# Kernel tuning notes

Measured on AMD Instinct MI355X. Metric: run time of the kernel, lower is better.

Reference implementation:

```python
import jax, jax.numpy as jnp
import numpy as np

K = 2  # top-k experts per token


def setup_inputs() -> dict:
    key = jax.random.key(0)
    k1, k2 = jax.random.split(key)
    B, T, D, E = 4, 4096, 4096, 64
    x = jax.random.normal(k1, (B, T, D), dtype=jnp.float32)
    W = jax.random.normal(k2, (E, D), dtype=jnp.float32) * (1.0 / np.sqrt(D))
    return {"x": x, "W": W}


def reference(x, W):
    # router_logits: [B, T, E]  (nn.Linear with no bias: x @ W.T)
    router_logits = jnp.einsum('btd,ed->bte', x, W)
    # top-k over expert dim, then softmax over the k selected logits
    topk_logits, topk_idx = jax.lax.top_k(router_logits, K)  # [B,T,K]
    topk_weight = jax.nn.softmax(topk_logits, axis=-1)       # [B,T,K]
    return (topk_idx, topk_weight, router_logits)
```

## Files before the change

### kernel.cpp

```cpp
#include <hip/hip_runtime.h>
#include <math.h>

#define NTOK 16384
#define DDIM 4096
#define NEXP 64
#define TAU  2e-4f
#define WS_LO 262144
#define NCW  32

typedef short bf16x8 __attribute__((ext_vector_type(8)));
typedef float f32x4  __attribute__((ext_vector_type(4)));

__device__ __forceinline__ unsigned short bf16_rne(float f) {
  unsigned u = __float_as_uint(f);
  u += 0x7fffu + ((u >> 16) & 1u);
  return (unsigned short)(u >> 16);
}

__device__ __forceinline__ void split4(float4 v, uint2& hi, uint2& lo) {
  unsigned h0 = bf16_rne(v.x), h1 = bf16_rne(v.y), h2 = bf16_rne(v.z), h3 = bf16_rne(v.w);
  float r0 = v.x - __uint_as_float(h0 << 16);
  float r1 = v.y - __uint_as_float(h1 << 16);
  float r2 = v.z - __uint_as_float(h2 << 16);
  float r3 = v.w - __uint_as_float(h3 << 16);
  unsigned l0 = bf16_rne(r0), l1 = bf16_rne(r1), l2 = bf16_rne(r2), l3 = bf16_rne(r3);
  hi = make_uint2(h0 | (h1 << 16), h2 | (h3 << 16));
  lo = make_uint2(l0 | (l1 << 16), l2 | (l3 << 16));
}

__device__ __forceinline__ void split4v(f32x4 v, uint2& hi, uint2& lo) {
  unsigned h0 = bf16_rne(v[0]), h1 = bf16_rne(v[1]), h2 = bf16_rne(v[2]), h3 = bf16_rne(v[3]);
  float r0 = v[0] - __uint_as_float(h0 << 16);
  float r1 = v[1] - __uint_as_float(h1 << 16);
  float r2 = v[2] - __uint_as_float(h2 << 16);
  float r3 = v[3] - __uint_as_float(h3 << 16);
  unsigned l0 = bf16_rne(r0), l1 = bf16_rne(r1), l2 = bf16_rne(r2), l3 = bf16_rne(r3);
  hi = make_uint2(h0 | (h1 << 16), h2 | (h3 << 16));
  lo = make_uint2(l0 | (l1 << 16), l2 | (l3 << 16));
}

__device__ __forceinline__ bf16x8 mk8(uint2 a, uint2 b) {
  union { uint4 u; bf16x8 v; } t;
  t.u = make_uint4(a.x, a.y, b.x, b.y);
  return t.v;
}

__device__ __forceinline__ void gld_lds16(const float* g, char* l) {
  __builtin_amdgcn_global_load_lds((const __attribute__((address_space(1))) void*)g,
                                   (__attribute__((address_space(3))) void*)l,
                                   16, 0, 0);
}

__device__ __forceinline__ bool better(float va, int ia, float vb, int ib) {
  return (va > vb) || (va == vb && ia < ib);
}
__device__ __forceinline__ bool betterd(double va, int ia, double vb, int ib) {
  return (va > vb) || (va == vb && ia < ib);
}
#define CE(va, ia, vb, ib) { if (better(vb, ib, va, ia)) { float _tv = va; va = vb; vb = _tv; int _ti = ia; ia = ib; ib = _ti; } }

__global__ __launch_bounds__(256)
void presplit_w(const float* __restrict__ w, short* __restrict__ ws) {
  const int tid = blockIdx.x * 256 + threadIdx.x;
  const int e = tid >> 9;
  const int o = tid & 511;
  const int c = o >> 2, q = o & 3;
  const int l = (e & 15) + 16 * q;
  const int g = e >> 4;
  const float* src = w + (size_t)e * DDIM + o * 8;
  float4 v0 = *(const float4*)src;
  float4 v1 = *(const float4*)(src + 4);
  uint2 h0, s0, h1, s1;
  split4(v0, h0, s0);
  split4(v1, h1, s1);
  const int off = c * 2048 + g * 512 + l * 8;
  *(uint4*)(ws + off)         = make_uint4(h0.x, h0.y, h1.x, h1.y);
  *(uint4*)(ws + WS_LO + off) = make_uint4(s0.x, s0.y, s1.x, s1.y);
}

__device__ __noinline__ void fixup_token(const float* __restrict__ x,
                                         const float* __restrict__ wgt,
                                         float* __restrict__ out_idx,
                                         float* __restrict__ out_wt,
                                         int tok, unsigned pk, int l) {
  const int e0 = pk & 255, e1 = (pk >> 8) & 255, e2 = (pk >> 16) & 255, e3 = (pk >> 24) & 255;
  const float* xr = x   + (size_t)tok * DDIM + l * 64;
  const float* w0 = wgt + (size_t)e0 * DDIM + l * 64;
  const float* w1 = wgt + (size_t)e1 * DDIM + l * 64;
  const float* w2 = wgt + (size_t)e2 * DDIM + l * 64;
  const float* w3 = wgt + (size_t)e3 * DDIM + l * 64;
  double s0 = 0.0, s1 = 0.0, s2 = 0.0, s3 = 0.0;
#pragma unroll 4
  for (int j = 0; j < 64; j += 4) {
    float4 xv = *(const float4*)(xr + j);
    float4 av = *(const float4*)(w0 + j);
    s0 = fma((double)xv.x, (double)av.x, s0); s0 = fma((double)xv.y, (double)av.y, s0);
    s0 = fma((double)xv.z, (double)av.z, s0); s0 = fma((double)xv.w, (double)av.w, s0);
    av = *(const float4*)(w1 + j);
    s1 = fma((double)xv.x, (double)av.x, s1); s1 = fma((double)xv.y, (double)av.y, s1);
    s1 = fma((double)xv.z, (double)av.z, s1); s1 = fma((double)xv.w, (double)av.w, s1);
    av = *(const float4*)(w2 + j);
    s2 = fma((double)xv.x, (double)av.x, s2); s2 = fma((double)xv.y, (double)av.y, s2);
    s2 = fma((double)xv.z, (double)av.z, s2); s2 = fma((double)xv.w, (double)av.w, s2);
    av = *(const float4*)(w3 + j);
    s3 = fma((double)xv.x, (double)av.x, s3); s3 = fma((double)xv.y, (double)av.y, s3);
    s3 = fma((double)xv.z, (double)av.z, s3); s3 = fma((double)xv.w, (double)av.w, s3);
  }
#pragma unroll
  for (int m = 1; m < 64; m <<= 1) {
    s0 += __shfl_xor(s0, m);
    s1 += __shfl_xor(s1, m);
    s2 += __shfl_xor(s2, m);
    s3 += __shfl_xor(s3, m);
  }
  if (l == 0) {
    double v0 = s0, v1 = s1, v2 = s2, v3 = s3;
    int i0 = e0, i1 = e1, i2 = e2, i3 = e3;
    if (betterd(v1, i1, v0, i0)) { double tv = v0; v0 = v1; v1 = tv; int ti = i0; i0 = i1; i1 = ti; }
    if (betterd(v3, i3, v2, i2)) { double tv = v2; v2 = v3; v3 = tv; int ti = i2; i2 = i3; i3 = ti; }
    if (betterd(v2, i2, v0, i0)) { double tv = v0; v0 = v2; v2 = tv; int ti = i0; i0 = i2; i2 = ti; }
    if (betterd(v3, i3, v1, i1)) { double tv = v1; v1 = v3; v3 = tv; int ti = i1; i1 = i3; i3 = ti; }
    if (betterd(v2, i2, v1, i1)) { double tv = v1; v1 = v2; v2 = tv; int ti = i1; i1 = i2; i2 = ti; }
    double ex = exp(v1 - v0);
    double den = 1.0 + ex;
    out_idx[tok * 2 + 0] = (float)i0;
    out_idx[tok * 2 + 1] = (float)i1;
    out_wt[tok * 2 + 0]  = (float)(1.0 / den);
    out_wt[tok * 2 + 1]  = (float)(ex / den);
  }
}

__global__ __launch_bounds__(256, 3)
void router_main(const float* __restrict__ x, const float* __restrict__ wgt,
                 const short* __restrict__ ws, float* __restrict__ out) {
  __shared__ __align__(16) char ldsbuf[32768];

  const int u = threadIdx.x;
  const int l = u & 63;
  const int wid = u >> 6;
  const int tokBase = blockIdx.x * 16;

  char* ring = ldsbuf + wid * 8192;
  const unsigned ldsbase =
      (unsigned)(size_t)(__attribute__((address_space(3))) char*)&ldsbuf[0];
  const unsigned rbase = ldsbase + wid * 8192 + l * 16;

  const int P = (blockIdx.x * 13) & 31;
#define PHYS(T) (((T) + P) & 31)

  const float* xbA = x + (size_t)(tokBase + (l & 15)) * DDIM + wid * 1024 + (l >> 4) * 8;
  const float* xbB = xbA + 4;

  const short* wch = ws + wid * 65536 + l * 8;

  f32x4 acc0 = {0,0,0,0}, acc1 = {0,0,0,0}, acc2 = {0,0,0,0}, acc3 = {0,0,0,0};
  bf16x8 wset[2][8];

#define LDW(SET, CC)                                                           \
  { asm volatile("" ::: "memory");                                             \
    wset[SET][0] = *(const bf16x8*)(wch + (CC) * 2048 + 0 * 512);              \
    wset[SET][1] = *(const bf16x8*)(wch + WS_LO + (CC) * 2048 + 0 * 512);      \
    wset[SET][2] = *(const bf16x8*)(wch + (CC) * 2048 + 1 * 512);              \
    wset[SET][3] = *(const bf16x8*)(wch + WS_LO + (CC) * 2048 + 1 * 512);      \
    wset[SET][4] = *(const bf16x8*)(wch + (CC) * 2048 + 2 * 512);              \
    wset[SET][5] = *(const bf16x8*)(wch + WS_LO + (CC) * 2048 + 2 * 512);      \
    wset[SET][6] = *(const bf16x8*)(wch + (CC) * 2048 + 3 * 512);              \
    wset[SET][7] = *(const bf16x8*)(wch + WS_LO + (CC) * 2048 + 3 * 512);      \
    asm volatile("" ::: "memory"); }

#define XISSUE(T, SLOT)                                                        \
  { const int cx_ = ((T) < NCW) ? (T) : NCW - 1;                               \
    const int cp_ = PHYS(cx_) * 32;                                            \
    char* d_ = ring + (SLOT) * 2048;                                           \
    gld_lds16(xbA + cp_, d_);                                                  \
    gld_lds16(xbB + cp_, d_ + 1024); }

#define MM(G, SET)                                                             \
  acc##G = __builtin_amdgcn_mfma_f32_16x16x32_bf16(ahi, wset[SET][2*(G)],   acc##G, 0, 0, 0); \
  acc##G = __builtin_amdgcn_mfma_f32_16x16x32_bf16(ahi, wset[SET][2*(G)+1], acc##G, 0, 0, 0); \
  acc##G = __builtin_amdgcn_mfma_f32_16x16x32_bf16(alo, wset[SET][2*(G)],   acc##G, 0, 0, 0);

#define STEP(T, SLOT, SET)                                                     \
  {                                                                            \
    asm volatile("" ::: "memory");                                             \
    XISSUE((T) + 3, ((T) + 3) & 3)                                             \
    asm volatile("s_waitcnt vmcnt(14)" ::: "memory");                          \
    {                                                                          \
      f32x4 f0, f1;                                                            \
      unsigned a_ = rbase + (SLOT) * 2048;                                     \
      asm volatile("ds_read_b128 %0, %2\n\tds_read_b128 %1, %2 offset:1024"    \
                   : "=&v"(f0), "=&v"(f1) : "v"(a_));                          \
      asm volatile("s_waitcnt lgkmcnt(0)" ::: "memory");                       \
      __builtin_amdgcn_sched_barrier(0);                                       \
      uint2 h0_, s0_, h1_, s1_;                                                \
      split4v(f0, h0_, s0_); split4v(f1, h1_, s1_);                            \
      bf16x8 ahi = mk8(h0_, h1_), alo = mk8(s0_, s1_);                         \
      MM(0, SET) MM(1, SET) MM(2, SET) MM(3, SET)                              \
    }                                                                          \
    { const int cw_ = ((T) + 2 < NCW) ? (T) + 2 : NCW - 1;                     \
      LDW(SET, PHYS(cw_)) }                                                    \
  }

  XISSUE(0, 0)
  LDW(0, PHYS(0))
  XISSUE(1, 1)
  LDW(1, PHYS(1))
  XISSUE(2, 2)

  for (int t = 0; t < NCW; t += 4) {
    STEP(t + 0, 0, 0)
    STEP(t + 1, 1, 1)
    STEP(t + 2, 2, 0)
    STEP(t + 3, 3, 1)
  }

  __syncthreads();
  float* p = (float*)ldsbuf;
#define PIDX(KQ, G, R) (((((KQ) * 4 + (G)) * 4 + (R)) << 6) + l)
  {
#pragma unroll
    for (int r = 0; r < 4; ++r) {
      p[PIDX(wid, 0, r)] = acc0[r];
      p[PIDX(wid, 1, r)] = acc1[r];
      p[PIDX(wid, 2, r)] = acc2[r];
      p[PIDX(wid, 3, r)] = acc3[r];
    }
  }
  __syncthreads();

  float* out_idx = out;
  float* out_wt  = out + NTOK * 2;
  float* out_lg  = out + NTOK * 4;

  float v0 = p[PIDX(0, 0, wid)] + p[PIDX(1, 0, wid)] + p[PIDX(2, 0, wid)] + p[PIDX(3, 0, wid)];
  float v1 = p[PIDX(0, 1, wid)] + p[PIDX(1, 1, wid)] + p[PIDX(2, 1, wid)] + p[PIDX(3, 1, wid)];
  float v2 = p[PIDX(0, 2, wid)] + p[PIDX(1, 2, wid)] + p[PIDX(2, 2, wid)] + p[PIDX(3, 2, wid)];
  float v3 = p[PIDX(0, 3, wid)] + p[PIDX(1, 3, wid)] + p[PIDX(2, 3, wid)] + p[PIDX(3, 3, wid)];

  const int tok = tokBase + (l >> 4) * 4 + wid;
  {
    float* dst = out_lg + (size_t)tok * NEXP + (l & 15);
    dst[0]  = v0;
    dst[16] = v1;
    dst[32] = v2;
    dst[48] = v3;
  }

  const int cbase = (l & 15);
  int i0 = cbase, i1 = cbase + 16, i2 = cbase + 32, i3 = cbase + 48;
  CE(v0, i0, v1, i1) CE(v2, i2, v3, i3) CE(v0, i0, v2, i2) CE(v1, i1, v3, i3) CE(v1, i1, v2, i2)
#pragma unroll
  for (int m = 1; m <= 8; m <<= 1) {
    float p0 = __shfl_xor(v0, m), p1 = __shfl_xor(v1, m);
    float p2 = __shfl_xor(v2, m), p3 = __shfl_xor(v3, m);
    int j0 = __shfl_xor(i0, m), j1 = __shfl_xor(i1, m);
    int j2 = __shfl_xor(i2, m), j3 = __shfl_xor(i3, m);
    CE(v0, i0, p3, j3) CE(v1, i1, p2, j2) CE(v2, i2, p1, j1) CE(v3, i3, p0, j0)
    CE(v0, i0, v2, i2) CE(v1, i1, v3, i3) CE(v0, i0, v1, i1) CE(v2, i2, v3, i3)
  }

  bool flag = false;
  unsigned pk = 0;
  if (cbase == 0) {
    flag = (v0 - v1 < TAU) || (v1 - v2 < TAU) || (v2 - v3 < TAU);
    pk = (unsigned)i0 | ((unsigned)i1 << 8) | ((unsigned)i2 << 16) | ((unsigned)i3 << 24);
    if (!flag) {
      float ex = expf(v1 - v0);
      float den = 1.0f + ex;
      out_idx[tok * 2 + 0] = (float)i0;
      out_idx[tok * 2 + 1] = (float)i1;
      out_wt[tok * 2 + 0]  = 1.0f / den;
      out_wt[tok * 2 + 1]  = ex / den;
    }
  }
  unsigned long long mk = __ballot(flag);
  while (mk) {
    const int src = __builtin_ctzll(mk);
    mk &= mk - 1;
    const unsigned pks = (unsigned)__shfl((int)pk, src);
    fixup_token(x, wgt, out_idx, out_wt, tokBase + (src >> 4) * 4 + wid, pks, l);
  }
}

extern "C" void kernel_launch(void* const* d_in, const int* in_sizes, int n_in,
                              void* d_out, int out_size, void* d_ws, size_t ws_size,
                              hipStream_t stream) {
  const float* x = (const float*)d_in[0];
  const float* w = (const float*)d_in[1];
  float* out = (float*)d_out;
  short* ws = (short*)d_ws;

  hipLaunchKernelGGL(presplit_w, dim3(128), dim3(256), 0, stream, w, ws);
  hipLaunchKernelGGL(router_main, dim3(NTOK / 16), dim3(256), 0, stream, x, w, ws, out);
}
```

Measured before the change: 103.1 us.

## Process 64 tokens per block to reuse weight fragments across four token tiles

Result: faster. 91.29 us (-11.4%).

```diff
diff --git a/kernel.cpp b/kernel.cpp
--- a/kernel.cpp
+++ b/kernel.cpp
@@ -130,155 +130,181 @@
   }
 }
 
-__global__ __launch_bounds__(256, 3)
+__global__ __launch_bounds__(256, 2)
 void router_main(const float* __restrict__ x, const float* __restrict__ wgt,
                  const short* __restrict__ ws, float* __restrict__ out) {
-  __shared__ __align__(16) char ldsbuf[32768];
+  __shared__ __align__(16) char ldsbuf[65536];
 
   const int u = threadIdx.x;
   const int l = u & 63;
   const int wid = u >> 6;
-  const int tokBase = blockIdx.x * 16;
-
-  char* ring = ldsbuf + wid * 8192;
+  const int tokBase = blockIdx.x * 64;
+
+  char* ring = ldsbuf + wid * 16384;
   const unsigned ldsbase =
       (unsigned)(size_t)(__attribute__((address_space(3))) char*)&ldsbuf[0];
-  const unsigned rbase = ldsbase + wid * 8192 + l * 16;
+  const unsigned rbase = ldsbase + wid * 16384 + l * 16;
 
   const int P = (blockIdx.x * 13) & 31;
 #define PHYS(T) (((T) + P) & 31)
 
-  const float* xbA = x + (size_t)(tokBase + (l & 15)) * DDIM + wid * 1024 + (l >> 4) * 8;
-  const float* xbB = xbA + 4;
+  const float* xA0 = x + (size_t)(tokBase +  0 + (l & 15)) * DDIM + wid * 1024 + (l >> 4) * 8;
+  const float* xB0 = xA0 + 4;
+  const float* xA1 = x + (size_t)(tokBase + 16 + (l & 15)) * DDIM + wid * 1024 + (l >> 4) * 8;
+  const float* xB1 = xA1 + 4;
+  const float* xA2 = x + (size_t)(tokBase + 32 + (l & 15)) * DDIM + wid * 1024 + (l >> 4) * 8;
+  const float* xB2 = xA2 + 4;
+  const float* xA3 = x + (size_t)(tokBase + 48 + (l & 15)) * DDIM + wid * 1024 + (l >> 4) * 8;
+  const float* xB3 = xA3 + 4;
 
   const short* wch = ws + wid * 65536 + l * 8;
 
-  f32x4 acc0 = {0,0,0,0}, acc1 = {0,0,0,0}, acc2 = {0,0,0,0}, acc3 = {0,0,0,0};
+  f32x4 acc[4][4];
+#pragma unroll
+  for (int t2 = 0; t2 < 4; ++t2)
+#pragma unroll
+    for (int g = 0; g < 4; ++g) acc[t2][g] = (f32x4){0.f, 0.f, 0.f, 0.f};
+
   bf16x8 wset[2][8];
 
-#define LDW(SET, CC)                                                           \
-  { asm volatile("" ::: "memory");                                             \
-    wset[SET][0] = *(const bf16x8*)(wch + (CC) * 2048 + 0 * 512);              \
-    wset[SET][1] = *(const bf16x8*)(wch + WS_LO + (CC) * 2048 + 0 * 512);      \
-    wset[SET][2] = *(const bf16x8*)(wch + (CC) * 2048 + 1 * 512);              \
-    wset[SET][3] = *(const bf16x8*)(wch + WS_LO + (CC) * 2048 + 1 * 512);      \
-    wset[SET][4] = *(const bf16x8*)(wch + (CC) * 2048 + 2 * 512);              \
-    wset[SET][5] = *(const bf16x8*)(wch + WS_LO + (CC) * 2048 + 2 * 512);      \
-    wset[SET][6] = *(const bf16x8*)(wch + (CC) * 2048 + 3 * 512);              \
-    wset[SET][7] = *(const bf16x8*)(wch + WS_LO + (CC) * 2048 + 3 * 512);      \
+#define LDW(SET, T)                                                            \
+  { const int cw_ = ((T) < NCW) ? (T) : NCW - 1;                               \
+    const int cc_ = PHYS(cw_);                                                 \
+    asm volatile("" ::: "memory");                                             \
+    wset[SET][0] = *(const bf16x8*)(wch + cc_ * 2048 + 0 * 512);               \
+    wset[SET][1] = *(const bf16x8*)(wch + WS_LO + cc_ * 2048 + 0 * 512);       \
+    wset[SET][2] = *(const bf16x8*)(wch + cc_ * 2048 + 1 * 512);               \
+    wset[SET][3] = *(const bf16x8*)(wch + WS_LO + cc_ * 2048 + 1 * 512);       \
+    wset[SET][4] = *(const bf16x8*)(wch + cc_ * 2048 + 2 * 512);               \
+    wset[SET][5] = *(const bf16x8*)(wch + WS_LO + cc_ * 2048 + 2 * 512);       \
+    wset[SET][6] = *(const bf16x8*)(wch + cc_ * 2048 + 3 * 512);               \
+    wset[SET][7] = *(const bf16x8*)(wch + WS_LO + cc_ * 2048 + 3 * 512);       \
     asm volatile("" ::: "memory"); }
 
 #define XISSUE(T, SLOT)                                                        \
   { const int cx_ = ((T) < NCW) ? (T) : NCW - 1;                               \
     const int cp_ = PHYS(cx_) * 32;                                            \
-    char* d_ = ring + (SLOT) * 2048;                                           \
-    gld_lds16(xbA + cp_, d_);                                                  \
-    gld_lds16(xbB + cp_, d_ + 1024); }
-
-#define MM(G, SET)                                                             \
-  acc##G = __builtin_amdgcn_mfma_f32_16x16x32_bf16(ahi, wset[SET][2*(G)],   acc##G, 0, 0, 0); \
-  acc##G = __builtin_amdgcn_mfma_f32_16x16x32_bf16(ahi, wset[SET][2*(G)+1], acc##G, 0, 0, 0); \
-  acc##G = __builtin_amdgcn_mfma_f32_16x16x32_bf16(alo, wset[SET][2*(G)],   acc##G, 0, 0, 0);
+    char* d_ = ring + (SLOT) * 8192;                                           \
+    gld_lds16(xA0 + cp_, d_);                                                  \
+    gld_lds16(xB0 + cp_, d_ + 1024);                                           \
+    gld_lds16(xA1 + cp_, d_ + 2048);                                           \
+    gld_lds16(xB1 + cp_, d_ + 3072);                                           \
+    gld_lds16(xA2 + cp_, d_ + 4096);                                           \
+    gld_lds16(xB2 + cp_, d_ + 5120);                                           \
+    gld_lds16(xA3 + cp_, d_ + 6144);                                           \
+    gld_lds16(xB3 + cp_, d_ + 7168); }
+
+#define MM(T2, G, SET)                                                         \
+  acc[T2][G] = __builtin_amdgcn_mfma_f32_16x16x32_bf16(ahi, wset[SET][2*(G)],   acc[T2][G], 0, 0, 0); \
+  acc[T2][G] = __builtin_amdgcn_mfma_f32_16x16x32_bf16(ahi, wset[SET][2*(G)+1], acc[T2][G], 0, 0, 0); \
+  acc[T2][G] = __builtin_amdgcn_mfma_f32_16x16x32_bf16(alo, wset[SET][2*(G)],   acc[T2][G], 0, 0, 0);
+
+#define COMPT(T2, SET, F0, F1)                                                 \
+  { uint2 h0_, s0_, h1_, s1_;                                                  \
+    split4v(F0, h0_, s0_); split4v(F1, h1_, s1_);                              \
+    bf16x8 ahi = mk8(h0_, h1_), alo = mk8(s0_, s1_);                           \
+    MM(T2, 0, SET) MM(T2, 1, SET) MM(T2, 2, SET) MM(T2, 3, SET) }
 
 #define STEP(T, SLOT, SET)                                                     \
   {                                                                            \
-    asm volatile("" ::: "memory");                                             \
-    XISSUE((T) + 3, ((T) + 3) & 3)                                             \
-    asm volatile("s_waitcnt vmcnt(14)" ::: "memory");                          \
-    {                                                                          \
-      f32x4 f0, f1;                                                            \
-      unsigned a_ = rbase + (SLOT) * 2048;                                     \
+    asm volatile("s_waitcnt vmcnt(16)" ::: "memory");                          \
+    f32x4 f0, f1, f2, f3, f4, f5, f6, f7;                                      \
+    { unsigned a_ = rbase + (SLOT) * 8192;                                     \
       asm volatile("ds_read_b128 %0, %2\n\tds_read_b128 %1, %2 offset:1024"    \
                    : "=&v"(f0), "=&v"(f1) : "v"(a_));                          \
-      asm volatile("s_waitcnt lgkmcnt(0)" ::: "memory");                       \
-      __builtin_amdgcn_sched_barrier(0);                                       \
-      uint2 h0_, s0_, h1_, s1_;                                                \
-      split4v(f0, h0_, s0_); split4v(f1, h1_, s1_);                            \
-      bf16x8 ahi = mk8(h0_, h1_), alo = mk8(s0_, s1_);                         \
-      MM(0, SET) MM(1, SET) MM(2, SET) MM(3, SET)                              \
-    }                                                                          \
-    { const int cw_ = ((T) + 2 < NCW) ? (T) + 2 : NCW - 1;                     \
-      LDW(SET, PHYS(cw_)) }                                                    \
+      asm volatile("ds_read_b128 %0, %2 offset:2048\n\tds_read_b128 %1, %2 offset:3072" \
+                   : "=&v"(f2), "=&v"(f3) : "v"(a_));                          \
+      asm volatile("ds_read_b128 %0, %2 offset:4096\n\tds_read_b128 %1, %2 offset:5120" \
+                   : "=&v"(f4), "=&v"(f5) : "v"(a_));                          \
+      asm volatile("ds_read_b128 %0, %2 offset:6144\n\tds_read_b128 %1, %2 offset:7168" \
+                   : "=&v"(f6), "=&v"(f7) : "v"(a_)); }                        \
+    asm volatile("s_waitcnt lgkmcnt(0)" ::: "memory");                         \
+    __builtin_amdgcn_sched_barrier(0);                                         \
+    XISSUE((T) + 2, SLOT)                                                      \
+    asm volatile("" ::: "memory");                                             \
+    COMPT(0, SET, f0, f1)                                                      \
+    COMPT(1, SET, f2, f3)                                                      \
+    COMPT(2, SET, f4, f5)                                                      \
+    COMPT(3, SET, f6, f7)                                                      \
+    LDW(SET, (T) + 2)                                                          \
   }
 
   XISSUE(0, 0)
-  LDW(0, PHYS(0))
+  LDW(0, 0)
   XISSUE(1, 1)
-  LDW(1, PHYS(1))
-  XISSUE(2, 2)
-
-  for (int t = 0; t < NCW; t += 4) {
-    STEP(t + 0, 0, 0)
+  LDW(1, 1)
+
+  for (int t = 0; t < NCW; t += 2) {
+    STEP(t, 0, 0)
     STEP(t + 1, 1, 1)
-    STEP(t + 2, 2, 0)
-    STEP(t + 3, 3, 1)
   }
 
   __syncthreads();
   float* p = (float*)ldsbuf;
-#define PIDX(KQ, G, R) (((((KQ) * 4 + (G)) * 4 + (R)) << 6) + l)
-  {
-#pragma unroll
-    for (int r = 0; r < 4; ++r) {
-      p[PIDX(wid, 0, r)] = acc0[r];
-      p[PIDX(wid, 1, r)] = acc1[r];
-      p[PIDX(wid, 2, r)] = acc2[r];
-      p[PIDX(wid, 3, r)] = acc3[r];
-    }
-  }
+#define PIDX(KQ, T2, G, R) ((((((KQ) * 4 + (T2)) * 4 + (G)) * 4 + (R)) << 6) + l)
+#pragma unroll
+  for (int t2 = 0; t2 < 4; ++t2)
+#pragma unroll
+    for (int g = 0; g < 4; ++g)
+#pragma unroll
+      for (int r = 0; r < 4; ++r)
+        p[PIDX(wid, t2, g, r)] = acc[t2][g][r];
   __syncthreads();
 
   float* out_idx = out;
   float* out_wt  = out + NTOK * 2;
   float* out_lg  = out + NTOK * 4;
 
-  float v0 = p[PIDX(0, 0, wid)] + p[PIDX(1, 0, wid)] + p[PIDX(2, 0, wid)] + p[PIDX(3, 0, wid)];
-  float v1 = p[PIDX(0, 1, wid)] + p[PIDX(1, 1, wid)] + p[PIDX(2, 1, wid)] + p[PIDX(3, 1, wid)];
-  float v2 = p[PIDX(0, 2, wid)] + p[PIDX(1, 2, wid)] + p[PIDX(2, 2, wid)] + p[PIDX(3, 2, wid)];
-  float v3 = p[PIDX(0, 3, wid)] + p[PIDX(1, 3, wid)] + p[PIDX(2, 3, wid)] + p[PIDX(3, 3, wid)];
-
-  const int tok = tokBase + (l >> 4) * 4 + wid;
-  {
-    float* dst = out_lg + (size_t)tok * NEXP + (l & 15);
-    dst[0]  = v0;
-    dst[16] = v1;
-    dst[32] = v2;
-    dst[48] = v3;
-  }
-
-  const int cbase = (l & 15);
-  int i0 = cbase, i1 = cbase + 16, i2 = cbase + 32, i3 = cbase + 48;
-  CE(v0, i0, v1, i1) CE(v2, i2, v3, i3) CE(v0, i0, v2, i2) CE(v1, i1, v3, i3) CE(v1, i1, v2, i2)
-#pragma unroll
-  for (int m = 1; m <= 8; m <<= 1) {
-    float p0 = __shfl_xor(v0, m), p1 = __shfl_xor(v1, m);
-    float p2 = __shfl_xor(v2, m), p3 = __shfl_xor(v3, m);
-    int j0 = __shfl_xor(i0, m), j1 = __shfl_xor(i1, m);
-    int j2 = __shfl_xor(i2, m), j3 = __shfl_xor(i3, m);
-    CE(v0, i0, p3, j3) CE(v1, i1, p2, j2) CE(v2, i2, p1, j1) CE(v3, i3, p0, j0)
-    CE(v0, i0, v2, i2) CE(v1, i1, v3, i3) CE(v0, i0, v1, i1) CE(v2, i2, v3, i3)
-  }
-
-  bool flag = false;
-  unsigned pk = 0;
-  if (cbase == 0) {
-    flag = (v0 - v1 < TAU) || (v1 - v2 < TAU) || (v2 - v3 < TAU);
-    pk = (unsigned)i0 | ((unsigned)i1 << 8) | ((unsigned)i2 << 16) | ((unsigned)i3 << 24);
-    if (!flag) {
-      float ex = expf(v1 - v0);
-      float den = 1.0f + ex;
-      out_idx[tok * 2 + 0] = (float)i0;
-      out_idx[tok * 2 + 1] = (float)i1;
-      out_wt[tok * 2 + 0]  = 1.0f / den;
-      out_wt[tok * 2 + 1]  = ex / den;
+#pragma unroll
+  for (int t2 = 0; t2 < 4; ++t2) {
+    float v0 = p[PIDX(0, t2, 0, wid)] + p[PIDX(1, t2, 0, wid)] + p[PIDX(2, t2, 0, wid)] + p[PIDX(3, t2, 0, wid)];
+    float v1 = p[PIDX(0, t2, 1, wid)] + p[PIDX(1, t2, 1, wid)] + p[PIDX(2, t2, 1, wid)] + p[PIDX(3, t2, 1, wid)];
+    float v2 = p[PIDX(0, t2, 2, wid)] + p[PIDX(1, t2, 2, wid)] + p[PIDX(2, t2, 2, wid)] + p[PIDX(3, t2, 2, wid)];
+    float v3 = p[PIDX(0, t2, 3, wid)] + p[PIDX(1, t2, 3, wid)] + p[PIDX(2, t2, 3, wid)] + p[PIDX(3, t2, 3, wid)];
+
+    const int tok = tokBase + t2 * 16 + (l >> 4) * 4 + wid;
+    {
+      float* dst = out_lg + (size_t)tok * NEXP + (l & 15);
+      dst[0]  = v0;
+      dst[16] = v1;
+      dst[32] = v2;
+      dst[48] = v3;
     }
-  }
-  unsigned long long mk = __ballot(flag);
-  while (mk) {
-    const int src = __builtin_ctzll(mk);
-    mk &= mk - 1;
-    const unsigned pks = (unsigned)__shfl((int)pk, src);
-    fixup_token(x, wgt, out_idx, out_wt, tokBase + (src >> 4) * 4 + wid, pks, l);
+
+    const int cbase = (l & 15);
+    int i0 = cbase, i1 = cbase + 16, i2 = cbase + 32, i3 = cbase + 48;
+    CE(v0, i0, v1, i1) CE(v2, i2, v3, i3) CE(v0, i0, v2, i2) CE(v1, i1, v3, i3) CE(v1, i1, v2, i2)
+#pragma unroll
+    for (int m = 1; m <= 8; m <<= 1) {
+      float p0 = __shfl_xor(v0, m), p1 = __shfl_xor(v1, m);
+      float p2 = __shfl_xor(v2, m), p3 = __shfl_xor(v3, m);
+      int j0 = __shfl_xor(i0, m), j1 = __shfl_xor(i1, m);
+      int j2 = __shfl_xor(i2, m), j3 = __shfl_xor(i3, m);
+      CE(v0, i0, p3, j3) CE(v1, i1, p2, j2) CE(v2, i2, p1, j1) CE(v3, i3, p0, j0)
+      CE(v0, i0, v2, i2) CE(v1, i1, v3, i3) CE(v0, i0, v1, i1) CE(v2, i2, v3, i3)
+    }
+
+    bool flag = false;
+    unsigned pk = 0;
+    if (cbase == 0) {
+      flag = (v0 - v1 < TAU) || (v1 - v2 < TAU) || (v2 - v3 < TAU);
+      pk = (unsigned)i0 | ((unsigned)i1 << 8) | ((unsigned)i2 << 16) | ((unsigned)i3 << 24);
+      if (!flag) {
+        float ex = expf(v1 - v0);
+        float den = 1.0f + ex;
+        out_idx[tok * 2 + 0] = (float)i0;
+        out_idx[tok * 2 + 1] = (float)i1;
+        out_wt[tok * 2 + 0]  = 1.0f / den;
+        out_wt[tok * 2 + 1]  = ex / den;
+      }
+    }
+    unsigned long long mk = __ballot(flag);
+    while (mk) {
+      const int src = __builtin_ctzll(mk);
+      mk &= mk - 1;
+      const unsigned pks = (unsigned)__shfl((int)pk, src);
+      fixup_token(x, wgt, out_idx, out_wt, tokBase + t2 * 16 + (src >> 4) * 4 + wid, pks, l);
+    }
   }
 }
 
@@ -291,5 +317,5 @@
   short* ws = (short*)d_ws;
 
   hipLaunchKernelGGL(presplit_w, dim3(128), dim3(256), 0, stream, w, ws);
-  hipLaunchKernelGGL(router_main, dim3(NTOK / 16), dim3(256), 0, stream, x, w, ws, out);
-}
+  hipLaunchKernelGGL(router_main, dim3(NTOK / 64), dim3(256), 0, stream, x, w, ws, out);
+}
```
